# Optimization experiments

Hardware: AMD Instinct MI355X
Metric: run time of the kernel (lower is better)

The kernel has to match this reference:

```python
import jax, jax.numpy as jnp
import numpy as np

N, F, H, C, E = 100000, 512, 3, 7, 3200000


def setup_inputs() -> dict:
    key = jax.random.key(0)
    k = jax.random.split(key, 6)
    x = jax.random.normal(k[0], (N, F), dtype=jnp.float32)
    src = jax.random.randint(k[1], (E,), 0, N)
    dst = jax.random.randint(k[2], (E,), 0, N)
    edge_index = jnp.stack([src, dst]).astype(jnp.int64)
    W_gcn = jax.random.normal(k[3], (F, H), dtype=jnp.float32) * (1.0 / np.sqrt(F))
    b_gcn = jnp.zeros((H,), dtype=jnp.float32)
    W_out = jax.random.normal(k[4], (H, C), dtype=jnp.float32) * (1.0 / np.sqrt(H))
    b_out = jnp.zeros((C,), dtype=jnp.float32)
    return {"x": x, "edge_index": edge_index, "W_gcn": W_gcn, "b_gcn": b_gcn,
            "W_out": W_out, "b_out": b_out}


def reference(x, edge_index, W_gcn, b_gcn, W_out, b_out):
    n = x.shape[0]
    # add self loops (PyG GCNConv default)
    loop = jnp.arange(n, dtype=edge_index.dtype)
    src = jnp.concatenate([edge_index[0], loop])  # [E+N]
    dst = jnp.concatenate([edge_index[1], loop])
    # symmetric normalization: deg at target, norm = d^-1/2[src] * d^-1/2[dst]
    deg = jax.ops.segment_sum(jnp.ones_like(dst, dtype=x.dtype), dst, num_segments=n)
    dis = jnp.where(deg > 0, jax.lax.rsqrt(deg), 0.0)
    norm = dis[src] * dis[dst]  # [E+N]
    # linear transform (no bias), then gather-scale-scatter aggregation
    xw = x @ W_gcn                              # [N, H]
    msgs = xw[src] * norm[:, None]              # [E+N, H]
    agg = jax.ops.segment_sum(msgs, dst, num_segments=n) + b_gcn  # [N, H]
    h = jax.nn.relu(agg)
    z = h @ W_out + b_out                       # [N, C]
    return (h, z)
```

## Files before the change

### kernel.cpp

```cpp
#include <hip/hip_runtime.h>

#define NF 512
#define NH 3
#define NC 7
#define RB 128
#define RBS 7
#define G1 256
#define NBMAX 1024
#define LDSCAP 8192


__device__ __forceinline__ int load_idx(const void* base, long long i, int is32) {
    return is32 ? ((const int*)base)[i] : (int)((const long long*)base)[i];
}

__device__ __forceinline__ int detect_is32(const int* __restrict__ ei, int E, int* anynz) {
    if (threadIdx.x == 0) *anynz = 0;
    __syncthreads();
    int lim = E < 2048 ? E : 2048;
    int nz = 0;
    for (int i = threadIdx.x; i < lim; i += blockDim.x) nz |= ei[2 * i + 1];
    if (nz) atomicOr(anynz, 1);
    __syncthreads();
    return *anynz;
}

__device__ __forceinline__ void gemm_rows(const float* __restrict__ x, const float* __restrict__ W,
                                          float* __restrict__ y4f, int row0, int row1,
                                          int wid, int nwaves) {
    int lane = threadIdx.x & 63;
    float4 w4[6];
    const float4* wp = (const float4*)W;
#pragma unroll
    for (int j = 0; j < 6; ++j) w4[j] = wp[lane * 6 + j];
    const float* wf = (const float*)w4;
    for (int row = row0 + wid; row < row1; row += nwaves) {
        const float4* xp = (const float4*)(x + (size_t)row * NF) + lane * 2;
        float4 a = xp[0], b = xp[1];
        float xv[8] = {a.x, a.y, a.z, a.w, b.x, b.y, b.z, b.w};
        float s0 = 0.f, s1 = 0.f, s2 = 0.f;
#pragma unroll
        for (int j = 0; j < 8; ++j) {
            s0 += xv[j] * wf[j * 3 + 0];
            s1 += xv[j] * wf[j * 3 + 1];
            s2 += xv[j] * wf[j * 3 + 2];
        }
#pragma unroll
        for (int off = 32; off; off >>= 1) {
            s0 += __shfl_down(s0, off);
            s1 += __shfl_down(s1, off);
            s2 += __shfl_down(s2, off);
        }
        if (lane == 0) {
            *(float2*)(y4f + 4 * (size_t)row) = make_float2(s0, s1);
            y4f[4 * (size_t)row + 2] = s2;
        }
    }
}


__global__ __launch_bounds__(256) void k_histgemm(const void* __restrict__ ei, int* __restrict__ hist,
                                                  int E, int NBv,
                                                  const float* __restrict__ x, const float* __restrict__ W,
                                                  float* __restrict__ y4f, int row1) {
    __shared__ int cnt[NBMAX];
    __shared__ int anynz;
    if (blockIdx.x < G1) {
        int is32 = detect_is32((const int*)ei, E, &anynz);
        for (int i = threadIdx.x; i < NBv; i += 256) cnt[i] = 0;
        __syncthreads();
        int EB = (E + G1 - 1) / G1;
        int e0 = blockIdx.x * EB;
        int e1 = min(E, e0 + EB);
        for (int i = e0 + threadIdx.x; i < e1; i += 256) {
            int d = load_idx(ei, (long long)E + i, is32);
            atomicAdd(&cnt[d >> RBS], 1);
        }
        __syncthreads();
        for (int b = threadIdx.x; b < NBv; b += 256)
            hist[b * G1 + blockIdx.x] = cnt[b];
    } else {
        int gb = gridDim.x - G1;
        gemm_rows(x, W, y4f, 0, row1, (blockIdx.x - G1) * 4 + (threadIdx.x >> 6), gb * 4);
    }
}

__global__ __launch_bounds__(256) void k_scangemm(int* __restrict__ hist, int* __restrict__ bcount,
                                                  int NBv,
                                                  const float* __restrict__ x, const float* __restrict__ W,
                                                  float* __restrict__ y4f, int row1, int row2) {
    __shared__ int wsum[4];
    if (blockIdx.x < (unsigned)NBv) {
        int b = blockIdx.x;
        int t = threadIdx.x, lane = t & 63, w = t >> 6;
        int v = hist[b * G1 + t];
        int incl = v;
#pragma unroll
        for (int off = 1; off < 64; off <<= 1) {
            int tt = __shfl_up(incl, off);
            if (lane >= off) incl += tt;
        }
        if (lane == 63) wsum[w] = incl;
        __syncthreads();
        int p = 0;
        for (int j = 0; j < w; ++j) p += wsum[j];
        hist[b * G1 + t] = p + incl - v;
        if (t == 255) bcount[b] = p + incl;
    } else {
        int gb = gridDim.x - NBv;
        gemm_rows(x, W, y4f, row1, row2, (blockIdx.x - NBv) * 4 + (threadIdx.x >> 6), gb * 4);
    }
}

__global__ __launch_bounds__(256) void k_sortgemm(const void* __restrict__ ei,
                                                  const int* __restrict__ hist,
                                                  const int* __restrict__ bcount,
                                                  int* __restrict__ bstart,
                                                  unsigned* __restrict__ recs, int E, int NBv,
                                                  const float* __restrict__ x, const float* __restrict__ W,
                                                  float* __restrict__ y4f, int row2, int row3) {
    __shared__ int bst[NBMAX];
    __shared__ int cur[NBMAX];
    __shared__ int wsum[4];
    __shared__ int anynz;
    if (blockIdx.x < G1) {
        int is32 = detect_is32((const int*)ei, E, &anynz);
        int t = threadIdx.x, lane = t & 63, w = t >> 6;
        int b4 = t * 4;
        int v[4];
        int s = 0;
#pragma unroll
        for (int j = 0; j < 4; ++j) {
            v[j] = (b4 + j < NBv) ? ((bcount[b4 + j] + 3) & ~3) : 0;
            s += v[j];
        }
        int incl = s;
#pragma unroll
        for (int off = 1; off < 64; off <<= 1) {
            int tt = __shfl_up(incl, off);
            if (lane >= off) incl += tt;
        }
        if (lane == 63) wsum[w] = incl;
        __syncthreads();
        int p = 0;
        for (int j = 0; j < w; ++j) p += wsum[j];
        int run = p + incl - s;
#pragma unroll
        for (int j = 0; j < 4; ++j) {
            if (b4 + j < NBMAX) bst[b4 + j] = run;
            run += v[j];
        }
        __syncthreads();
        for (int b = t; b < NBv; b += 256)
            cur[b] = bst[b] + hist[b * G1 + blockIdx.x];
        if (blockIdx.x == 0)
            for (int b = t; b < NBv; b += 256) bstart[b] = bst[b];
        __syncthreads();
        int EB = (E + G1 - 1) / G1;
        int e0 = blockIdx.x * EB;
        int e1 = min(E, e0 + EB);
        for (int i = e0 + t; i < e1; i += 256) {
            int sv = load_idx(ei, i, is32);
            int d = load_idx(ei, (long long)E + i, is32);
            int b = d >> RBS;
            int pos = atomicAdd(&cur[b], 1);
            recs[pos] = ((unsigned)(d & (RB - 1)) << 17) | (unsigned)sv;
        }
    } else {
        int gb = gridDim.x - G1;
        gemm_rows(x, W, y4f, row2, row3, (blockIdx.x - G1) * 4 + (threadIdx.x >> 6), gb * 4);
    }
}

__global__ __launch_bounds__(256) void k_deggemm(const unsigned* __restrict__ recs,
                                                 const int* __restrict__ bstart, const int* __restrict__ bcount,
                                                 float* __restrict__ y4f, int* __restrict__ rs,
                                                 int n, int NBv,
                                                 const float* __restrict__ x, const float* __restrict__ W,
                                                 int row3) {
    __shared__ int cnt[RB];
    if (blockIdx.x < (unsigned)NBv) {
        int t = threadIdx.x;
        for (int i = t; i < RB; i += 256) cnt[i] = 0;
        __syncthreads();
        int b = blockIdx.x;
        int s0 = bstart[b], s1 = s0 + bcount[b];
        for (int i = s0 + t; i < s1; i += 256)
            atomicAdd(&cnt[recs[i] >> 17], 1);
        __syncthreads();
        int rbase = b << RBS;
        for (int r = t; r < RB; r += 256) {
            int row = rbase + r;
            if (row < n) y4f[4 * (size_t)row + 3] = rsqrtf((float)(cnt[r] + 1));
        }
        if (t < 64) {
            int cA = cnt[2 * t], cB = cnt[2 * t + 1];
            int s = cA + cB;
            int incl = s;
#pragma unroll
            for (int off = 1; off < 64; off <<= 1) {
                int tt = __shfl_up(incl, off);
                if (t >= off) incl += tt;
            }
            int ex = s0 + incl - s;
            int* rsb = rs + (size_t)b * (RB + 1);
            rsb[2 * t] = ex;
            rsb[2 * t + 1] = ex + cA;
            if (t == 63) rsb[RB] = ex + s;
        }
    } else {
        int gb = gridDim.x - NBv;
        gemm_rows(x, W, y4f, row3, n, (blockIdx.x - NBv) * 4 + (threadIdx.x >> 6), gb * 4);
    }
}

__global__ __launch_bounds__(256) void k_aggrow(const unsigned* __restrict__ recs,
                                                const int* __restrict__ bstart, const int* __restrict__ bcount,
                                                const int* __restrict__ rs,
                                                const float4* __restrict__ y4, const float* __restrict__ bg,
                                                const float* __restrict__ Wo, const float* __restrict__ bo,
                                                float* __restrict__ outH, float* __restrict__ outZ, int n) {
    __shared__ int cnt[RB];
    __shared__ int cur[RB];
    __shared__ int rsl[RB + 1];
    __shared__ int lrec[LDSCAP];
    int b = blockIdx.x, t = threadIdx.x;
    int grp = t >> 3, sub = t & 7;
    int s0 = bstart[b], cntb = bcount[b];
    float acc[4][3] = {{0.f, 0.f, 0.f}, {0.f, 0.f, 0.f}, {0.f, 0.f, 0.f}, {0.f, 0.f, 0.f}};
    if (cntb <= LDSCAP) {
        const int* rsb = rs + (size_t)b * (RB + 1);
        for (int i = t; i <= RB; i += 256) {
            int v = rsb[i] - s0;
            rsl[i] = v;
            if (i < RB) cur[i] = v;
        }
        __syncthreads();
        for (int i = s0 + t; i < s0 + cntb; i += 256) {
            unsigned rec = recs[i];
            int pos = atomicAdd(&cur[rec >> 17], 1);
            lrec[pos] = (int)(rec & 0x1FFFF);
        }
        __syncthreads();
#pragma unroll
        for (int k = 0; k < 4; ++k) {
            int rr = grp + k * 32;
            int e0 = rsl[rr], e1 = rsl[rr + 1];
            for (int i = e0 + sub; i < e1; i += 8) {
                float4 v = y4[lrec[i]];
                acc[k][0] += v.w * v.x;
                acc[k][1] += v.w * v.y;
                acc[k][2] += v.w * v.z;
            }
        }
    } else {
        for (int c0 = s0; c0 < s0 + cntb; c0 += LDSCAP) {
            int c1 = min(s0 + cntb, c0 + LDSCAP);
            for (int i = t; i < RB; i += 256) cnt[i] = 0;
            __syncthreads();
            for (int i = c0 + t; i < c1; i += 256)
                atomicAdd(&cnt[recs[i] >> 17], 1);
            __syncthreads();
            if (t < 64) {
                int cA = cnt[2 * t], cB = cnt[2 * t + 1];
                int s = cA + cB;
                int incl = s;
#pragma unroll
                for (int off = 1; off < 64; off <<= 1) {
                    int tt = __shfl_up(incl, off);
                    if (t >= off) incl += tt;
                }
                int ex = incl - s;
                rsl[2 * t] = ex;
                rsl[2 * t + 1] = ex + cA;
                cur[2 * t] = ex;
                cur[2 * t + 1] = ex + cA;
                if (t == 63) rsl[RB] = ex + s;
            }
            __syncthreads();
            for (int i = c0 + t; i < c1; i += 256) {
                unsigned rec = recs[i];
                int pos = atomicAdd(&cur[rec >> 17], 1);
                lrec[pos] = (int)(rec & 0x1FFFF);
            }
            __syncthreads();
#pragma unroll
            for (int k = 0; k < 4; ++k) {
                int rr = grp + k * 32;
                int e0 = rsl[rr], e1 = rsl[rr + 1];
                for (int i = e0 + sub; i < e1; i += 8) {
                    float4 v = y4[lrec[i]];
                    acc[k][0] += v.w * v.x;
                    acc[k][1] += v.w * v.y;
                    acc[k][2] += v.w * v.z;
                }
            }
            __syncthreads();
        }
    }
    float b0 = bg[0], b1 = bg[1], b2 = bg[2];
    int rbase = b << RBS;
#pragma unroll
    for (int k = 0; k < 4; ++k) {
        float a0 = acc[k][0], a1 = acc[k][1], a2 = acc[k][2];
#pragma unroll
        for (int o = 4; o; o >>= 1) {
            a0 += __shfl_xor(a0, o);
            a1 += __shfl_xor(a1, o);
            a2 += __shfl_xor(a2, o);
        }
        if (sub == 0) {
            int row = rbase + grp + k * 32;
            if (row < n) {
                float4 yv = y4[row];
                float di = yv.w;
                float h0 = fmaxf(di * (a0 + di * yv.x) + b0, 0.f);
                float h1 = fmaxf(di * (a1 + di * yv.y) + b1, 0.f);
                float h2 = fmaxf(di * (a2 + di * yv.z) + b2, 0.f);
                outH[row * 3 + 0] = h0; outH[row * 3 + 1] = h1; outH[row * 3 + 2] = h2;
#pragma unroll
                for (int c = 0; c < NC; ++c)
                    outZ[row * NC + c] = h0 * Wo[c] + h1 * Wo[NC + c] + h2 * Wo[2 * NC + c] + bo[c];
            }
        }
    }
}


__global__ void k_detect_fb(const int* ei, int* flag, int E) {
    __shared__ int anynz;
    if (threadIdx.x == 0) anynz = 0;
    __syncthreads();
    int lim = E < 2048 ? E : 2048;
    int nz = 0;
    for (int i = threadIdx.x; i < lim; i += blockDim.x) nz |= ei[2 * i + 1];
    if (nz) atomicOr(&anynz, 1);
    __syncthreads();
    if (threadIdx.x == 0) *flag = anynz;
}
__global__ void k_init_fb(float* deg, int n) {
    int i = blockIdx.x * blockDim.x + threadIdx.x;
    if (i < n) deg[i] = 1.0f;
}
__global__ void k_degc_fb(const void* ei, const int* flag, float* deg, int E, int n) {
    int i = blockIdx.x * blockDim.x + threadIdx.x;
    if (i >= E) return;
    int d = load_idx(ei, (long long)E + i, *flag);
    if ((unsigned)d < (unsigned)n) atomicAdd(&deg[d], 1.0f);
}
__global__ __launch_bounds__(256) void k_gemm_fb(const float* x, const float* W, float* degdis,
                                                 float* xw, float* agg, int n) {
    __shared__ float wl[NF * NH];
    for (int j = threadIdx.x; j < NF * NH; j += 256) wl[j] = W[j];
    __syncthreads();
    int row = blockIdx.x * 4 + (threadIdx.x >> 6);
    if (row >= n) return;
    int lane = threadIdx.x & 63;
    const float4* xp = (const float4*)(x + (size_t)row * NF + lane * 8);
    float4 a = xp[0], b = xp[1];
    float xv[8] = {a.x, a.y, a.z, a.w, b.x, b.y, b.z, b.w};
    float s0 = 0.f, s1 = 0.f, s2 = 0.f;
    int f0 = lane * 8;
#pragma unroll
    for (int j = 0; j < 8; ++j) {
        float v = xv[j];
        const float* wp = &wl[(f0 + j) * NH];
        s0 += v * wp[0]; s1 += v * wp[1]; s2 += v * wp[2];
    }
#pragma unroll
    for (int off = 32; off; off >>= 1) {
        s0 += __shfl_down(s0, off); s1 += __shfl_down(s1, off); s2 += __shfl_down(s2, off);
    }
    if (lane == 0) {
        float d = degdis[row];
        float di = d > 0.f ? rsqrtf(d) : 0.f;
        degdis[row] = di;
        xw[row * 3 + 0] = s0; xw[row * 3 + 1] = s1; xw[row * 3 + 2] = s2;
        float n2 = di * di;
        agg[row * 3 + 0] = s0 * n2; agg[row * 3 + 1] = s1 * n2; agg[row * 3 + 2] = s2 * n2;
    }
}
__global__ void k_scat_fb(const void* ei, const int* flag, const float* dis, const float* xw,
                          float* agg, int E, int n) {
    int i = blockIdx.x * blockDim.x + threadIdx.x;
    if (i >= E) return;
    int is32 = *flag;
    int s = load_idx(ei, i, is32);
    int d = load_idx(ei, (long long)E + i, is32);
    if ((unsigned)s >= (unsigned)n || (unsigned)d >= (unsigned)n) return;
    float w = dis[s] * dis[d];
    atomicAdd(&agg[d * 3 + 0], xw[s * 3 + 0] * w);
    atomicAdd(&agg[d * 3 + 1], xw[s * 3 + 1] * w);
    atomicAdd(&agg[d * 3 + 2], xw[s * 3 + 2] * w);
}
__global__ void k_final_fb(const float* agg, const float* bg, const float* Wo, const float* bo,
                           float* outH, float* outZ, int n) {
    int i = blockIdx.x * blockDim.x + threadIdx.x;
    if (i >= n) return;
    float h0 = fmaxf(agg[i * 3 + 0] + bg[0], 0.f);
    float h1 = fmaxf(agg[i * 3 + 1] + bg[1], 0.f);
    float h2 = fmaxf(agg[i * 3 + 2] + bg[2], 0.f);
    outH[i * 3 + 0] = h0; outH[i * 3 + 1] = h1; outH[i * 3 + 2] = h2;
#pragma unroll
    for (int c = 0; c < NC; ++c)
        outZ[i * NC + c] = h0 * Wo[c] + h1 * Wo[NC + c] + h2 * Wo[2 * NC + c] + bo[c];
}


extern "C" void kernel_launch(void* const* d_in, const int* in_sizes, int n_in,
                              void* d_out, int out_size, void* d_ws, size_t ws_size,
                              hipStream_t stream) {
    const float* x  = (const float*)d_in[0];
    const void*  ei = d_in[1];
    const float* Wg = (const float*)d_in[2];
    const float* bg = (const float*)d_in[3];
    const float* Wo = (const float*)d_in[4];
    const float* bo = (const float*)d_in[5];

    const int N = in_sizes[0] / NF;
    const int E = in_sizes[1] / 2;
    const int NBv = (N + RB - 1) >> RBS;

    float* outH = (float*)d_out;
    float* outZ = outH + (size_t)3 * N;

    int*   wsI = (int*)d_ws;
    float* wsF = (float*)d_ws;

    size_t off = 64;
    int* hist   = wsI + off; off += (size_t)NBMAX * G1;
    int* bstart = wsI + off; off += NBMAX;
    int* bcount = wsI + off; off += NBMAX;
    int* rs     = wsI + off; off += (size_t)NBMAX * (RB + 1);
    off = (off + 3) & ~(size_t)3;
    float* y4   = wsF + off; off += (size_t)4 * N;
    unsigned* recs = (unsigned*)(wsI + off); off += (size_t)E + 4 * NBMAX;

    bool fast = (off * 4 <= ws_size) && (N <= 131072) && (NBv <= NBMAX);

    if (fast) {
        int r1 = (int)((long long)N * 30 / 100);
        int r2 = (int)((long long)N * 36 / 100);
        int r3 = (int)((long long)N * 80 / 100);
        k_histgemm<<<G1 + 512, dim3(256), 0, stream>>>(ei, hist, E, NBv, x, Wg, y4, r1);
        k_scangemm<<<NBv + 128, dim3(256), 0, stream>>>(hist, bcount, NBv, x, Wg, y4, r1, r2);
        k_sortgemm<<<G1 + 896, dim3(256), 0, stream>>>(ei, hist, bcount, bstart, recs, E, NBv,
                                                       x, Wg, y4, r2, r3);
        k_deggemm<<<NBv + 512, dim3(256), 0, stream>>>(recs, bstart, bcount, y4, rs,
                                                       N, NBv, x, Wg, r3);
        k_aggrow<<<NBv, dim3(256), 0, stream>>>(recs, bstart, bcount, rs, (const float4*)y4,
                                                bg, Wo, bo, outH, outZ, N);
    } else {
        int* flag  = wsI;
        float* deg = wsF + 64;
        float* xw  = deg + N;
        float* agg = xw + (size_t)3 * N;
        int gN = (N + 255) / 256, gE = (E + 255) / 256;
        dim3 blk(256);
        k_detect_fb<<<1, blk, 0, stream>>>((const int*)ei, flag, E);
        k_init_fb<<<gN, blk, 0, stream>>>(deg, N);
        k_degc_fb<<<gE, blk, 0, stream>>>(ei, flag, deg, E, N);
        k_gemm_fb<<<(N + 3) / 4, blk, 0, stream>>>(x, Wg, deg, xw, agg, N);
        k_scat_fb<<<gE, blk, 0, stream>>>(ei, flag, deg, xw, agg, E, N);
        k_final_fb<<<gN, blk, 0, stream>>>(agg, bg, Wo, bo, outH, outZ, N);
    }
}
```

Before: 113.1 us.

## Fold histogram scan kernel into sort kernel to remove a launch

New measurement: 220.8 us. 95.3% more time.

```diff
diff --git a/kernel.cpp b/kernel.cpp
--- a/kernel.cpp
+++ b/kernel.cpp
@@ -85,40 +85,14 @@
     }
 }
 
-__global__ __launch_bounds__(256) void k_scangemm(int* __restrict__ hist, int* __restrict__ bcount,
-                                                  int NBv,
+__global__ __launch_bounds__(256) void k_sortgemm(const void* __restrict__ ei,
+                                                  const int* __restrict__ hist,
+                                                  int* __restrict__ bstart, int* __restrict__ bcount,
+                                                  unsigned* __restrict__ recs, int E, int NBv,
                                                   const float* __restrict__ x, const float* __restrict__ W,
                                                   float* __restrict__ y4f, int row1, int row2) {
-    __shared__ int wsum[4];
-    if (blockIdx.x < (unsigned)NBv) {
-        int b = blockIdx.x;
-        int t = threadIdx.x, lane = t & 63, w = t >> 6;
-        int v = hist[b * G1 + t];
-        int incl = v;
-#pragma unroll
-        for (int off = 1; off < 64; off <<= 1) {
-            int tt = __shfl_up(incl, off);
-            if (lane >= off) incl += tt;
-        }
-        if (lane == 63) wsum[w] = incl;
-        __syncthreads();
-        int p = 0;
-        for (int j = 0; j < w; ++j) p += wsum[j];
-        hist[b * G1 + t] = p + incl - v;
-        if (t == 255) bcount[b] = p + incl;
-    } else {
-        int gb = gridDim.x - NBv;
-        gemm_rows(x, W, y4f, row1, row2, (blockIdx.x - NBv) * 4 + (threadIdx.x >> 6), gb * 4);
-    }
-}
-
-__global__ __launch_bounds__(256) void k_sortgemm(const void* __restrict__ ei,
-                                                  const int* __restrict__ hist,
-                                                  const int* __restrict__ bcount,
-                                                  int* __restrict__ bstart,
-                                                  unsigned* __restrict__ recs, int E, int NBv,
-                                                  const float* __restrict__ x, const float* __restrict__ W,
-                                                  float* __restrict__ y4f, int row2, int row3) {
+    __shared__ int tot[NBMAX];
+    __shared__ int pre[NBMAX];
     __shared__ int bst[NBMAX];
     __shared__ int cur[NBMAX];
     __shared__ int wsum[4];
@@ -126,12 +100,30 @@
     if (blockIdx.x < G1) {
         int is32 = detect_is32((const int*)ei, E, &anynz);
         int t = threadIdx.x, lane = t & 63, w = t >> 6;
+        int blk = blockIdx.x;
+        for (int b = w; b < NBv; b += 4) {
+            int sp = 0, st = 0;
+            const int* hb = &hist[b * G1];
+#pragma unroll
+            for (int g0 = 0; g0 < G1; g0 += 64) {
+                int v = hb[g0 + lane];
+                st += v;
+                if (g0 + lane < blk) sp += v;
+            }
+#pragma unroll
+            for (int o = 32; o; o >>= 1) {
+                st += __shfl_down(st, o);
+                sp += __shfl_down(sp, o);
+            }
+            if (lane == 0) { tot[b] = st; pre[b] = sp; }
+        }
+        __syncthreads();
         int b4 = t * 4;
         int v[4];
         int s = 0;
 #pragma unroll
         for (int j = 0; j < 4; ++j) {
-            v[j] = (b4 + j < NBv) ? ((bcount[b4 + j] + 3) & ~3) : 0;
+            v[j] = (b4 + j < NBv) ? ((tot[b4 + j] + 3) & ~3) : 0;
             s += v[j];
         }
         int incl = s;
@@ -152,12 +144,12 @@
         }
         __syncthreads();
         for (int b = t; b < NBv; b += 256)
-            cur[b] = bst[b] + hist[b * G1 + blockIdx.x];
-        if (blockIdx.x == 0)
-            for (int b = t; b < NBv; b += 256) bstart[b] = bst[b];
+            cur[b] = bst[b] + pre[b];
+        if (blk == 0)
+            for (int b = t; b < NBv; b += 256) { bstart[b] = bst[b]; bcount[b] = tot[b]; }
         __syncthreads();
         int EB = (E + G1 - 1) / G1;
-        int e0 = blockIdx.x * EB;
+        int e0 = blk * EB;
         int e1 = min(E, e0 + EB);
         for (int i = e0 + t; i < e1; i += 256) {
             int sv = load_idx(ei, i, is32);
@@ -168,7 +160,7 @@
         }
     } else {
         int gb = gridDim.x - G1;
-        gemm_rows(x, W, y4f, row2, row3, (blockIdx.x - G1) * 4 + (threadIdx.x >> 6), gb * 4);
+        gemm_rows(x, W, y4f, row1, row2, (blockIdx.x - G1) * 4 + (threadIdx.x >> 6), gb * 4);
     }
 }
 
@@ -177,7 +169,7 @@
                                                  float* __restrict__ y4f, int* __restrict__ rs,
                                                  int n, int NBv,
                                                  const float* __restrict__ x, const float* __restrict__ W,
-                                                 int row3) {
+                                                 int row2) {
     __shared__ int cnt[RB];
     if (blockIdx.x < (unsigned)NBv) {
         int t = threadIdx.x;
@@ -210,7 +202,7 @@
         }
     } else {
         int gb = gridDim.x - NBv;
-        gemm_rows(x, W, y4f, row3, n, (blockIdx.x - NBv) * 4 + (threadIdx.x >> 6), gb * 4);
+        gemm_rows(x, W, y4f, row2, n, (blockIdx.x - NBv) * 4 + (threadIdx.x >> 6), gb * 4);
     }
 }
 
@@ -439,15 +431,13 @@
     bool fast = (off * 4 <= ws_size) && (N <= 131072) && (NBv <= NBMAX);
 
     if (fast) {
-        int r1 = (int)((long long)N * 30 / 100);
-        int r2 = (int)((long long)N * 36 / 100);
-        int r3 = (int)((long long)N * 80 / 100);
+        int r1 = (int)((long long)N * 32 / 100);
+        int r2 = (int)((long long)N * 78 / 100);
         k_histgemm<<<G1 + 512, dim3(256), 0, stream>>>(ei, hist, E, NBv, x, Wg, y4, r1);
-        k_scangemm<<<NBv + 128, dim3(256), 0, stream>>>(hist, bcount, NBv, x, Wg, y4, r1, r2);
-        k_sortgemm<<<G1 + 896, dim3(256), 0, stream>>>(ei, hist, bcount, bstart, recs, E, NBv,
-                                                       x, Wg, y4, r2, r3);
+        k_sortgemm<<<G1 + 896, dim3(256), 0, stream>>>(ei, hist, bstart, bcount, recs, E, NBv,
+                                                       x, Wg, y4, r1, r2);
         k_deggemm<<<NBv + 512, dim3(256), 0, stream>>>(recs, bstart, bcount, y4, rs,
-                                                       N, NBv, x, Wg, r3);
+                                                       N, NBv, x, Wg, r2);
         k_aggrow<<<NBv, dim3(256), 0, stream>>>(recs, bstart, bcount, rs, (const float4*)y4,
                                                 bg, Wo, bo, outH, outZ, N);
     } else {
```
